# Kernel tuning notes

Measured on AMD Instinct MI355X. Metric: run time of the kernel, lower is better.

The kernel has to match this reference:

```python
import jax, jax.numpy as jnp
import numpy as np

DIM_IN, DIM_Q, DIM_V = 1024, 1024, 1024
B, S = 4, 2048
NEG_INF = 1.0e9


def setup_inputs() -> dict:
    key = jax.random.key(0)
    ks = jax.random.split(key, 11)
    c_q = (6.0 / (DIM_IN + DIM_Q)) ** 0.5
    c_v = (6.0 / (DIM_IN + DIM_V)) ** 0.5
    b_bound = 1.0 / np.sqrt(DIM_IN)  # torch Linear default bias init
    return {
        "query": jax.random.normal(ks[0], (B, S, DIM_IN), jnp.float32),
        "key": jax.random.normal(ks[1], (B, S, DIM_IN), jnp.float32),
        "value": jax.random.normal(ks[2], (B, S, DIM_IN), jnp.float32),
        "mask": jax.random.randint(ks[3], (B, S, S), 0, 2).astype(bool),
        "Wq": jax.random.uniform(ks[4], (DIM_Q, DIM_IN), jnp.float32, -c_q, c_q),
        "bq": jax.random.uniform(ks[5], (DIM_Q,), jnp.float32, -b_bound, b_bound),
        "Wk": jax.random.uniform(ks[6], (DIM_Q, DIM_IN), jnp.float32, -c_q, c_q),
        "bk": jax.random.uniform(ks[7], (DIM_Q,), jnp.float32, -b_bound, b_bound),
        "Wv": jax.random.uniform(ks[8], (DIM_V, DIM_IN), jnp.float32, -c_v, c_v),
        "bv": jax.random.uniform(ks[9], (DIM_V,), jnp.float32, -b_bound, b_bound),
    }


def reference(query, key, value, mask, Wq, bq, Wk, bk, Wv, bv):
    q = jnp.einsum("bsd,qd->bsq", query, Wq) + bq  # [B,S,dim_q]
    k = jnp.einsum("bsd,qd->bsq", key, Wk) + bk    # [B,S,dim_q]
    v = jnp.einsum("bsd,vd->bsv", value, Wv) + bv  # [B,S,dim_v]
    scale = 1.0 / jnp.sqrt(jnp.asarray(q.shape[-1], q.dtype))
    scores = jnp.einsum("bqd,bkd->bqk", q, k) * scale  # [B,S,S]
    scores = jnp.where(mask, -NEG_INF, scores)
    affinity = jax.nn.softmax(scores, axis=-1)
    out = jnp.einsum("bqk,bkv->bqv", affinity, v)  # [B,S,dim_v]
    return out
```

## Files before the change

kernel.cpp:

```cpp
#include <hip/hip_runtime.h>

#define BB 4
#define SS 2048
#define DD 1024

typedef __attribute__((ext_vector_type(8))) short short8;
typedef __attribute__((ext_vector_type(4))) float f32x4;

__device__ __forceinline__ unsigned short f2b(float f) {
  unsigned u = __builtin_bit_cast(unsigned, f);
  u += 0x7fffu + ((u >> 16) & 1u);
  return (unsigned short)(u >> 16);
}
__device__ __forceinline__ float b2f(unsigned short us) {
  unsigned u = (unsigned)us << 16;
  return __builtin_bit_cast(float, u);
}

__device__ __forceinline__ void gl2lds16(const void* g, void* l) {
  __builtin_amdgcn_global_load_lds(
      (__attribute__((address_space(1))) unsigned int*)(void*)(size_t)(uintptr_t)g,
      (__attribute__((address_space(3))) unsigned int*)l, 16, 0, 0);
}

__global__ __launch_bounds__(256) void cvt_all(
    const float* __restrict__ q, const float* __restrict__ k, const float* __restrict__ v,
    const float* __restrict__ wq, const float* __restrict__ wk, const float* __restrict__ wv,
    unsigned short* __restrict__ qo, unsigned short* __restrict__ ko, unsigned short* __restrict__ vo,
    unsigned short* __restrict__ wqo, unsigned short* __restrict__ wko, unsigned short* __restrict__ wvo) {
  const int z = blockIdx.z;
  const float* s;
  unsigned short* d;
  size_t i;
  if (blockIdx.x < 4096) {
    s = z == 0 ? q : (z == 1 ? k : v);
    d = z == 0 ? qo : (z == 1 ? ko : vo);
    i = (size_t)blockIdx.x * 2048 + threadIdx.x * 8;
  } else {
    s = z == 0 ? wq : (z == 1 ? wk : wv);
    d = z == 0 ? wqo : (z == 1 ? wko : wvo);
    i = (size_t)(blockIdx.x - 4096) * 2048 + threadIdx.x * 8;
  }
  float4 a = *(const float4*)(s + i);
  float4 b = *(const float4*)(s + i + 4);
  union { unsigned short us[8]; uint4 v4; } o;
  o.us[0] = f2b(a.x); o.us[1] = f2b(a.y); o.us[2] = f2b(a.z); o.us[3] = f2b(a.w);
  o.us[4] = f2b(b.x); o.us[5] = f2b(b.y); o.us[6] = f2b(b.z); o.us[7] = f2b(b.w);
  *(uint4*)(d + i) = o.v4;
}

enum { EPI_BIAS_COL = 0, EPI_BIAS_ROW = 1, EPI_SCORE = 2, EPI_OUT = 3 };

template <int EPI>
__global__ __launch_bounds__(256, 2) void gemm_bt(
    const unsigned short* __restrict__ A, int lda, long long aBatch,
    const unsigned short* __restrict__ Bm, int ldb, long long bBatch,
    void* __restrict__ Cv, int ldc, long long cBatch,
    int K,
    const float* __restrict__ bias,
    const float* __restrict__ bias2,
    float scale) {
  __shared__ unsigned short sA[128 * 32];
  __shared__ unsigned short sB[128 * 32];
  const int tid  = threadIdx.x;
  const int wave = tid >> 6;
  const int lane = tid & 63;
  const int l15  = lane & 15;
  const int quad = lane >> 4;
  const int waveR = wave >> 1, waveC = wave & 1;
  const int bm = blockIdx.x * 128;
  const int bn = blockIdx.y * 128;
  const int z  = blockIdx.z;
  A  += (long long)z * aBatch;
  Bm += (long long)z * bBatch;

  const unsigned short* gA0 = A  + (size_t)(bm + (tid >> 2)) * lda + (tid & 3) * 8;
  const unsigned short* gA1 = gA0 + (size_t)64 * lda;
  const unsigned short* gB0 = Bm + (size_t)(bn + (tid >> 2)) * ldb + (tid & 3) * 8;
  const unsigned short* gB1 = gB0 + (size_t)64 * ldb;
  unsigned short* lA = sA + wave * 64 * 8;
  unsigned short* lB = sB + wave * 64 * 8;

  f32x4 acc[4][4] = {};

  const int aro = (waveR * 64 + l15) * 32 + quad * 8;
  const int bro = (waveC * 64 + l15) * 32 + quad * 8;

  for (int kt = 0; kt < K; kt += 32) {
    gl2lds16(gA0, lA);
    gl2lds16(gA1, lA + 256 * 8);
    gl2lds16(gB0, lB);
    gl2lds16(gB1, lB + 256 * 8);
    gA0 += 32; gA1 += 32; gB0 += 32; gB1 += 32;
    __syncthreads();
    short8 af[4], bf[4];
#pragma unroll
    for (int i = 0; i < 4; ++i) af[i] = *(const short8*)(sA + aro + i * 16 * 32);
#pragma unroll
    for (int j = 0; j < 4; ++j) bf[j] = *(const short8*)(sB + bro + j * 16 * 32);
#pragma unroll
    for (int i = 0; i < 4; ++i)
#pragma unroll
      for (int j = 0; j < 4; ++j)
        acc[i][j] = __builtin_amdgcn_mfma_f32_16x16x32_bf16(af[i], bf[j], acc[i][j], 0, 0, 0);
    __syncthreads();
  }

  const int r0 = bm + waveR * 64 + quad * 4;
  const int c0 = bn + waveC * 64 + l15;

  if constexpr (EPI == EPI_SCORE) {
    unsigned short* Cz = (unsigned short*)Cv + (long long)z * cBatch;
#pragma unroll
    for (int i = 0; i < 4; ++i)
#pragma unroll
      for (int r = 0; r < 4; ++r) {
        int row = r0 + i * 16 + r;
#pragma unroll
        for (int j = 0; j < 4; ++j) {
          int col = c0 + j * 16;
          Cz[(size_t)row * ldc + col] = f2b(acc[i][j][r] * scale);
        }
      }
  } else if constexpr (EPI == EPI_OUT) {
    float* Cz = (float*)Cv + (long long)z * cBatch;
#pragma unroll
    for (int i = 0; i < 4; ++i)
#pragma unroll
      for (int r = 0; r < 4; ++r) {
        int row = r0 + i * 16 + r;
#pragma unroll
        for (int j = 0; j < 4; ++j) {
          int col = c0 + j * 16;
          Cz[(size_t)row * ldc + col] = acc[i][j][r];
        }
      }
  } else {
    const float* bp = (z == 0) ? bias : bias2;
    unsigned short* Cz = (unsigned short*)Cv + (long long)z * cBatch;
#pragma unroll
    for (int i = 0; i < 4; ++i)
#pragma unroll
      for (int r = 0; r < 4; ++r) {
        int row = r0 + i * 16 + r;
#pragma unroll
        for (int j = 0; j < 4; ++j) {
          int col = c0 + j * 16;
          float v = acc[i][j][r] + (EPI == EPI_BIAS_COL ? bp[col] : bp[row]);
          Cz[(size_t)row * ldc + col] = f2b(v);
        }
      }
  }
}

__global__ __launch_bounds__(256) void softmax_rows(const unsigned short* __restrict__ Sc,
                                                    const void* __restrict__ mask,
                                                    unsigned short* __restrict__ P) {
  const size_t r = blockIdx.x;
  const unsigned short* src = Sc + r * SS;
  unsigned short* dst = P + r * SS;
  const int tid = threadIdx.x;
  const int wave = tid >> 6, lane = tid & 63;
  __shared__ int anyv[4];
  __shared__ float red[8];

  unsigned pw = ((const unsigned*)mask)[tid];
  unsigned long long bal = __ballot(pw > 1u);
  if (lane == 0) anyv[wave] = (bal != 0ULL) ? 1 : 0;
  __syncthreads();
  const bool isU8 = (anyv[0] | anyv[1] | anyv[2] | anyv[3]) != 0;

  unsigned mbits = 0;
  if (isU8) {
    uint2 v = *(const uint2*)((const unsigned char*)mask + r * SS + tid * 8);
#pragma unroll
    for (int j = 0; j < 4; ++j) {
      mbits |= (((v.x >> (8 * j)) & 0xffu) ? 1u : 0u) << j;
      mbits |= (((v.y >> (8 * j)) & 0xffu) ? 1u : 0u) << (j + 4);
    }
  } else {
    const uint4* p = (const uint4*)((const int*)mask + r * SS + tid * 8);
    uint4 a = p[0], b = p[1];
    mbits = (a.x ? 1u : 0u) | ((a.y ? 1u : 0u) << 1) | ((a.z ? 1u : 0u) << 2) |
            ((a.w ? 1u : 0u) << 3) | ((b.x ? 1u : 0u) << 4) | ((b.y ? 1u : 0u) << 5) |
            ((b.z ? 1u : 0u) << 6) | ((b.w ? 1u : 0u) << 7);
  }

  union { unsigned short us[8]; uint4 v; } in;
  in.v = *(const uint4*)(src + tid * 8);
  float xs[8];
#pragma unroll
  for (int k = 0; k < 8; ++k)
    xs[k] = ((mbits >> k) & 1u) ? -1.0e9f : b2f(in.us[k]);
  float mx = xs[0];
#pragma unroll
  for (int k = 1; k < 8; ++k) mx = fmaxf(mx, xs[k]);
#pragma unroll
  for (int o = 32; o; o >>= 1) mx = fmaxf(mx, __shfl_xor(mx, o));
  if (lane == 0) red[wave] = mx;
  __syncthreads();
  mx = fmaxf(fmaxf(red[0], red[1]), fmaxf(red[2], red[3]));
  float e[8], s = 0.f;
#pragma unroll
  for (int k = 0; k < 8; ++k) { e[k] = __expf(xs[k] - mx); s += e[k]; }
#pragma unroll
  for (int o = 32; o; o >>= 1) s += __shfl_xor(s, o);
  if (lane == 0) red[4 + wave] = s;
  __syncthreads();
  s = (red[4] + red[5]) + (red[6] + red[7]);
  float inv = 1.0f / s;
  union { unsigned short us[8]; uint4 v; } o;
#pragma unroll
  for (int k = 0; k < 8; ++k) o.us[k] = f2b(e[k] * inv);
  *(uint4*)(dst + tid * 8) = o.v;
}

extern "C" void kernel_launch(void* const* d_in, const int* in_sizes, int n_in,
                              void* d_out, int out_size, void* d_ws, size_t ws_size,
                              hipStream_t stream) {
  const float* query = (const float*)d_in[0];
  const float* key   = (const float*)d_in[1];
  const float* value = (const float*)d_in[2];
  const void*  mask  = d_in[3];
  const float* Wq = (const float*)d_in[4];
  const float* bq = (const float*)d_in[5];
  const float* Wk = (const float*)d_in[6];
  const float* bk = (const float*)d_in[7];
  const float* Wv = (const float*)d_in[8];
  const float* bv = (const float*)d_in[9];
  float* out = (float*)d_out;

  char* ws = (char*)d_ws;
  const size_t MB = 1024 * 1024;
  unsigned short* qin = (unsigned short*)(ws + 0 * MB);
  unsigned short* kin = (unsigned short*)(ws + 16 * MB);
  unsigned short* vin = (unsigned short*)(ws + 32 * MB);
  unsigned short* Wqb = (unsigned short*)(ws + 48 * MB);
  unsigned short* Wkb = (unsigned short*)(ws + 50 * MB);
  unsigned short* Wvb = (unsigned short*)(ws + 52 * MB);
  unsigned short* qb  = (unsigned short*)(ws + 54 * MB);
  unsigned short* kb  = (unsigned short*)(ws + 70 * MB);
  unsigned short* vT  = (unsigned short*)(ws + 86 * MB);
  unsigned short* Sc  = (unsigned short*)(ws + 102 * MB);
  unsigned short* P   = (unsigned short*)(ws + 134 * MB);

  dim3 blk(256);

  cvt_all<<<dim3(4608, 1, 3), blk, 0, stream>>>(
      query, key, value, Wq, Wk, Wv, qin, kin, vin, Wqb, Wkb, Wvb);

  gemm_bt<EPI_BIAS_COL><<<dim3(64, 8, 2), blk, 0, stream>>>(
      qin, 1024, 8388608LL, Wqb, 1024, 1048576LL, qb, 1024, 8388608LL,
      1024, bq, bk, 0.f);

  gemm_bt<EPI_BIAS_ROW><<<dim3(8, 64, 1), blk, 0, stream>>>(
      Wvb, 1024, 0, vin, 1024, 0, vT, 8192, 0, 1024, bv, bv, 0.f);

  gemm_bt<EPI_SCORE><<<dim3(16, 16, BB), blk, 0, stream>>>(
      qb, 1024, (long long)SS * 1024, kb, 1024, (long long)SS * 1024,
      Sc, SS, (long long)SS * SS, 1024, nullptr, nullptr, 0.03125f);

  softmax_rows<<<dim3(BB * SS), blk, 0, stream>>>(Sc, mask, P);

  gemm_bt<EPI_OUT><<<dim3(16, 8, BB), blk, 0, stream>>>(
      P, SS, (long long)SS * SS, vT, 8192, (long long)SS,
      out, 1024, (long long)SS * 1024, SS, nullptr, nullptr, 1.f);
}
```

Before: 374.4 us.

## Replace 128x128 GEMM with double-buffered 256x256 tile kernel using swizzled LDS

Replaces the simple 128x128 bf16 MFMA GEMM, which syncs twice per 32-wide K step, with a 512-thread 256x256 tile kernel. It double-buffers 64-wide K tiles in 128KB of LDS, uses an XOR-swizzled LDS layout to avoid bank conflicts, and interleaves global-to-LDS staging with MFMA quadrants under explicit vmcnt waits, barriers and setprio. The goal is more data reuse per tile and overlap of memory loads with math. The cost is far fewer blocks per GEMM (for example 128 blocks for the QK projection), which may underfill the 256 CUs, plus heavy register use and 128KB of LDS per block.

```diff
diff --git a/kernel.cpp b/kernel.cpp
--- a/kernel.cpp
+++ b/kernel.cpp
@@ -51,105 +51,175 @@
 
 enum { EPI_BIAS_COL = 0, EPI_BIAS_ROW = 1, EPI_SCORE = 2, EPI_OUT = 3 };
 
+#define BAR() asm volatile("s_barrier" ::: "memory")
+#define VMW4() asm volatile("s_waitcnt vmcnt(4)" ::: "memory")
+#define VMW0() asm volatile("s_waitcnt vmcnt(0)" ::: "memory")
+
+#define MMA_QUAD(MH, NH)                                                       \
+  do {                                                                         \
+    __builtin_amdgcn_s_setprio(1);                                             \
+    _Pragma("unroll") for (int mt = 0; mt < 4; ++mt)                           \
+        _Pragma("unroll") for (int nt = 0; nt < 2; ++nt)                       \
+            _Pragma("unroll") for (int ks = 0; ks < 2; ++ks)                   \
+                acc[MH][NH][mt][nt] = __builtin_amdgcn_mfma_f32_16x16x32_bf16( \
+                    afr[mt][ks], bfr[nt][ks], acc[MH][NH][mt][nt], 0, 0, 0);   \
+    __builtin_amdgcn_s_setprio(0);                                             \
+  } while (0)
+
 template <int EPI>
-__global__ __launch_bounds__(256, 2) void gemm_bt(
+__global__ __launch_bounds__(512, 2) void gemm256(
     const unsigned short* __restrict__ A, int lda, long long aBatch,
     const unsigned short* __restrict__ Bm, int ldb, long long bBatch,
-    void* __restrict__ Cv, int ldc, long long cBatch,
-    int K,
+    void* __restrict__ Cv, int ldc, long long cBatch, int K,
     const float* __restrict__ bias,
     const float* __restrict__ bias2,
     float scale) {
-  __shared__ unsigned short sA[128 * 32];
-  __shared__ unsigned short sB[128 * 32];
-  const int tid  = threadIdx.x;
-  const int wave = tid >> 6;
-  const int lane = tid & 63;
-  const int l15  = lane & 15;
-  const int quad = lane >> 4;
-  const int waveR = wave >> 1, waveC = wave & 1;
-  const int bm = blockIdx.x * 128;
-  const int bn = blockIdx.y * 128;
-  const int z  = blockIdx.z;
-  A  += (long long)z * aBatch;
+  __shared__ __attribute__((aligned(128))) char lds[131072];
+  const int tid = threadIdx.x;
+  const int wave = tid >> 6, lane = tid & 63;
+  const int l15 = lane & 15, quad = lane >> 4;
+  const int wr = wave >> 2, wc = wave & 3;
+  const int bm = blockIdx.x * 256, bn = blockIdx.y * 256, z = blockIdx.z;
+  A += (long long)z * aBatch;
   Bm += (long long)z * bBatch;
 
-  const unsigned short* gA0 = A  + (size_t)(bm + (tid >> 2)) * lda + (tid & 3) * 8;
-  const unsigned short* gA1 = gA0 + (size_t)64 * lda;
-  const unsigned short* gB0 = Bm + (size_t)(bn + (tid >> 2)) * ldb + (tid & 3) * 8;
-  const unsigned short* gB1 = gB0 + (size_t)64 * ldb;
-  unsigned short* lA = sA + wave * 64 * 8;
-  unsigned short* lB = sB + wave * 64 * 8;
-
-  f32x4 acc[4][4] = {};
-
-  const int aro = (waveR * 64 + l15) * 32 + quad * 8;
-  const int bro = (waveC * 64 + l15) * 32 + quad * 8;
-
-  for (int kt = 0; kt < K; kt += 32) {
-    gl2lds16(gA0, lA);
-    gl2lds16(gA1, lA + 256 * 8);
-    gl2lds16(gB0, lB);
-    gl2lds16(gB1, lB + 256 * 8);
-    gA0 += 32; gA1 += 32; gB0 += 32; gB1 += 32;
-    __syncthreads();
-    short8 af[4], bf[4];
-#pragma unroll
-    for (int i = 0; i < 4; ++i) af[i] = *(const short8*)(sA + aro + i * 16 * 32);
-#pragma unroll
-    for (int j = 0; j < 4; ++j) bf[j] = *(const short8*)(sB + bro + j * 16 * 32);
-#pragma unroll
-    for (int i = 0; i < 4; ++i)
-#pragma unroll
-      for (int j = 0; j < 4; ++j)
-        acc[i][j] = __builtin_amdgcn_mfma_f32_16x16x32_bf16(af[i], bf[j], acc[i][j], 0, 0, 0);
-    __syncthreads();
-  }
-
-  const int r0 = bm + waveR * 64 + quad * 4;
-  const int c0 = bn + waveC * 64 + l15;
-
+  const int laneterm = l15 * 64 + ((quad * 16) ^ ((l15 & 8) << 2));
+
+  size_t aoff0, aoff1, boff0, boff1;
+  int dst0, dst1;
+  {
+    int s = tid, s2 = s ^ (((s >> 5) & 1) << 1);
+    int row = (s2 >> 7) * 16 + ((s2 >> 2) & 15);
+    int col = ((s2 >> 6) & 1) * 32 + (s2 & 3) * 8;
+    aoff0 = (size_t)(bm + row) * lda + col;
+    boff0 = (size_t)(bn + row) * ldb + col;
+    dst0 = (tid & ~63) * 16;
+    s = tid + 512; s2 = s ^ (((s >> 5) & 1) << 1);
+    row = (s2 >> 7) * 16 + ((s2 >> 2) & 15);
+    col = ((s2 >> 6) & 1) * 32 + (s2 & 3) * 8;
+    aoff1 = (size_t)(bm + row) * lda + col;
+    boff1 = (size_t)(bn + row) * ldb + col;
+    dst1 = (tid & ~63) * 16 + 8192;
+  }
+
+  auto stageA = [&](int buf, int half, int t) {
+    const unsigned short* s0 = A + aoff0 + (size_t)(half * 128) * lda + t * 64;
+    const unsigned short* s1 = A + aoff1 + (size_t)(half * 128) * lda + t * 64;
+    char* d = lds + buf * 65536 + half * 16384;
+    gl2lds16(s0, d + dst0);
+    gl2lds16(s1, d + dst1);
+  };
+  auto stageB = [&](int buf, int half, int t) {
+    const unsigned short* s0 = Bm + boff0 + (size_t)(half * 128) * ldb + t * 64;
+    const unsigned short* s1 = Bm + boff1 + (size_t)(half * 128) * ldb + t * 64;
+    char* d = lds + 32768 + buf * 65536 + half * 16384;
+    gl2lds16(s0, d + dst0);
+    gl2lds16(s1, d + dst1);
+  };
+
+  f32x4 acc[2][2][4][2] = {};
+  short8 afr[4][2], bfr[2][2];
+
+  auto loadA = [&](int buf, int mh) {
+    const char* rg = lds + buf * 65536 + mh * 16384;
+#pragma unroll
+    for (int mt = 0; mt < 4; ++mt)
+#pragma unroll
+      for (int ks = 0; ks < 2; ++ks)
+        afr[mt][ks] = *(const short8*)(rg + ((wr * 4 + mt) * 2 + ks) * 1024 + laneterm);
+  };
+  auto loadB = [&](int buf, int nh) {
+    const char* rg = lds + 32768 + buf * 65536 + nh * 16384;
+#pragma unroll
+    for (int nt = 0; nt < 2; ++nt)
+#pragma unroll
+      for (int ks = 0; ks < 2; ++ks)
+        bfr[nt][ks] = *(const short8*)(rg + ((wc * 2 + nt) * 2 + ks) * 1024 + laneterm);
+  };
+
+  const int NT = K >> 6;
+  const int NI = NT >> 1;
+
+  stageA(0, 0, 0); stageA(0, 1, 0); stageB(0, 0, 0); stageB(0, 1, 0);
+  stageA(1, 0, 1); stageB(1, 0, 1);
+  VMW4(); BAR();
+
+  for (int i = 0; i < NI - 1; ++i) {
+    const int t1 = 2 * i + 1;
+    loadA(0, 0); loadB(0, 0); stageA(1, 1, t1);              BAR(); MMA_QUAD(0, 0); BAR();
+    loadB(0, 1);              stageB(1, 1, t1);              BAR(); MMA_QUAD(0, 1); BAR();
+    loadA(0, 1); loadB(0, 0); stageA(0, 0, t1 + 1);          BAR(); MMA_QUAD(1, 0); BAR();
+    loadB(0, 1);              stageB(0, 0, t1 + 1); VMW4();  BAR(); MMA_QUAD(1, 1); BAR();
+    loadA(1, 0); loadB(1, 0); stageA(0, 1, t1 + 1);          BAR(); MMA_QUAD(0, 0); BAR();
+    loadB(1, 1);              stageB(0, 1, t1 + 1);          BAR(); MMA_QUAD(0, 1); BAR();
+    loadA(1, 1); loadB(1, 0); stageA(1, 0, t1 + 2);          BAR(); MMA_QUAD(1, 0); BAR();
+    loadB(1, 1);              stageB(1, 0, t1 + 2); VMW4();  BAR(); MMA_QUAD(1, 1); BAR();
+  }
+  {
+    const int t1 = NT - 1;
+    loadA(0, 0); loadB(0, 0); stageA(1, 1, t1);              BAR(); MMA_QUAD(0, 0); BAR();
+    loadB(0, 1);              stageB(1, 1, t1);              BAR(); MMA_QUAD(0, 1); BAR();
+    loadA(0, 1); loadB(0, 0);                                BAR(); MMA_QUAD(1, 0); BAR();
+    loadB(0, 1);                                    VMW0();  BAR(); MMA_QUAD(1, 1); BAR();
+    loadA(1, 0); loadB(1, 0);                                BAR(); MMA_QUAD(0, 0); BAR();
+    loadB(1, 1);                                             BAR(); MMA_QUAD(0, 1); BAR();
+    loadA(1, 1); loadB(1, 0);                                BAR(); MMA_QUAD(1, 0); BAR();
+    loadB(1, 1);                                             BAR(); MMA_QUAD(1, 1);
+  }
+
+  const int r0 = bm + wr * 64 + quad * 4;
+  const int c0 = bn + wc * 32 + l15;
   if constexpr (EPI == EPI_SCORE) {
     unsigned short* Cz = (unsigned short*)Cv + (long long)z * cBatch;
 #pragma unroll
-    for (int i = 0; i < 4; ++i)
-#pragma unroll
-      for (int r = 0; r < 4; ++r) {
-        int row = r0 + i * 16 + r;
-#pragma unroll
-        for (int j = 0; j < 4; ++j) {
-          int col = c0 + j * 16;
-          Cz[(size_t)row * ldc + col] = f2b(acc[i][j][r] * scale);
+    for (int mh = 0; mh < 2; ++mh)
+#pragma unroll
+      for (int mt = 0; mt < 4; ++mt)
+#pragma unroll
+        for (int r = 0; r < 4; ++r) {
+          const int row = r0 + mh * 128 + mt * 16 + r;
+#pragma unroll
+          for (int nh = 0; nh < 2; ++nh)
+#pragma unroll
+            for (int nt = 0; nt < 2; ++nt)
+              Cz[(size_t)row * ldc + c0 + nh * 128 + nt * 16] =
+                  f2b(acc[mh][nh][mt][nt][r] * scale);
         }
-      }
   } else if constexpr (EPI == EPI_OUT) {
     float* Cz = (float*)Cv + (long long)z * cBatch;
 #pragma unroll
-    for (int i = 0; i < 4; ++i)
-#pragma unroll
-      for (int r = 0; r < 4; ++r) {
-        int row = r0 + i * 16 + r;
-#pragma unroll
-        for (int j = 0; j < 4; ++j) {
-          int col = c0 + j * 16;
-          Cz[(size_t)row * ldc + col] = acc[i][j][r];
+    for (int mh = 0; mh < 2; ++mh)
+#pragma unroll
+      for (int mt = 0; mt < 4; ++mt)
+#pragma unroll
+        for (int r = 0; r < 4; ++r) {
+          const int row = r0 + mh * 128 + mt * 16 + r;
+#pragma unroll
+          for (int nh = 0; nh < 2; ++nh)
+#pragma unroll
+            for (int nt = 0; nt < 2; ++nt)
+              Cz[(size_t)row * ldc + c0 + nh * 128 + nt * 16] = acc[mh][nh][mt][nt][r];
         }
-      }
   } else {
     const float* bp = (z == 0) ? bias : bias2;
     unsigned short* Cz = (unsigned short*)Cv + (long long)z * cBatch;
 #pragma unroll
-    for (int i = 0; i < 4; ++i)
-#pragma unroll
-      for (int r = 0; r < 4; ++r) {
-        int row = r0 + i * 16 + r;
-#pragma unroll
-        for (int j = 0; j < 4; ++j) {
-          int col = c0 + j * 16;
-          float v = acc[i][j][r] + (EPI == EPI_BIAS_COL ? bp[col] : bp[row]);
-          Cz[(size_t)row * ldc + col] = f2b(v);
+    for (int mh = 0; mh < 2; ++mh)
+#pragma unroll
+      for (int mt = 0; mt < 4; ++mt)
+#pragma unroll
+        for (int r = 0; r < 4; ++r) {
+          const int row = r0 + mh * 128 + mt * 16 + r;
+#pragma unroll
+          for (int nh = 0; nh < 2; ++nh)
+#pragma unroll
+            for (int nt = 0; nt < 2; ++nt) {
+              const int col = c0 + nh * 128 + nt * 16;
+              float v = acc[mh][nh][mt][nt][r] +
+                        (EPI == EPI_BIAS_COL ? bp[col] : bp[row]);
+              Cz[(size_t)row * ldc + col] = f2b(v);
+            }
         }
-      }
   }
 }
 
@@ -244,25 +314,25 @@
   unsigned short* Sc  = (unsigned short*)(ws + 102 * MB);
   unsigned short* P   = (unsigned short*)(ws + 134 * MB);
 
-  dim3 blk(256);
+  dim3 blk(256), blk512(512);
 
   cvt_all<<<dim3(4608, 1, 3), blk, 0, stream>>>(
       query, key, value, Wq, Wk, Wv, qin, kin, vin, Wqb, Wkb, Wvb);
 
-  gemm_bt<EPI_BIAS_COL><<<dim3(64, 8, 2), blk, 0, stream>>>(
+  gemm256<EPI_BIAS_COL><<<dim3(32, 4, 2), blk512, 0, stream>>>(
       qin, 1024, 8388608LL, Wqb, 1024, 1048576LL, qb, 1024, 8388608LL,
       1024, bq, bk, 0.f);
 
-  gemm_bt<EPI_BIAS_ROW><<<dim3(8, 64, 1), blk, 0, stream>>>(
+  gemm256<EPI_BIAS_ROW><<<dim3(4, 32, 1), blk512, 0, stream>>>(
       Wvb, 1024, 0, vin, 1024, 0, vT, 8192, 0, 1024, bv, bv, 0.f);
 
-  gemm_bt<EPI_SCORE><<<dim3(16, 16, BB), blk, 0, stream>>>(
+  gemm256<EPI_SCORE><<<dim3(8, 8, BB), blk512, 0, stream>>>(
       qb, 1024, (long long)SS * 1024, kb, 1024, (long long)SS * 1024,
       Sc, SS, (long long)SS * SS, 1024, nullptr, nullptr, 0.03125f);
 
   softmax_rows<<<dim3(BB * SS), blk, 0, stream>>>(Sc, mask, P);
 
-  gemm_bt<EPI_OUT><<<dim3(16, 8, BB), blk, 0, stream>>>(
+  gemm256<EPI_OUT><<<dim3(8, 4, BB), blk512, 0, stream>>>(
       P, SS, (long long)SS * SS, vT, 8192, (long long)SS,
       out, 1024, (long long)SS * 1024, SS, nullptr, nullptr, 1.f);
 }
```

Result: faster. 365.1 us (-2.5%).

## Double-buffer GEMM LDS tiles and merge Q/K/V projections into one launch

Applied to the files above, without the earlier changes.

Turns the shared GEMM main loop into a two-stage LDS double buffer. The next K-tile's global-to-LDS loads are issued after the current fragments are read and before the MFMAs, with one barrier per iteration instead of two. The three projection GEMMs are also merged into a single proj_all launch so the V projection runs alongside Q and K. LDS use per block doubles, which may limit occupancy, and the correctness of the single-barrier scheme relies on the async load ordering.

```diff
diff --git a/kernel.cpp b/kernel.cpp
--- a/kernel.cpp
+++ b/kernel.cpp
@@ -49,65 +49,105 @@
   *(uint4*)(d + i) = o.v4;
 }
 
-enum { EPI_BIAS_COL = 0, EPI_BIAS_ROW = 1, EPI_SCORE = 2, EPI_OUT = 3 };
+#define GEMM_BODY(A_, lda_, B_, ldb_, KK)                                       \
+  __shared__ unsigned short sA[2][128 * 32];                                    \
+  __shared__ unsigned short sB[2][128 * 32];                                    \
+  const int tid  = threadIdx.x;                                                 \
+  const int wave = tid >> 6;                                                    \
+  const int lane = tid & 63;                                                    \
+  const int l15  = lane & 15;                                                   \
+  const int quad = lane >> 4;                                                   \
+  const int waveR = wave >> 1, waveC = wave & 1;                                \
+  const unsigned short* gA0 = A_ + (size_t)(bm + (tid >> 2)) * lda_ + (tid & 3) * 8; \
+  const unsigned short* gA1 = gA0 + (size_t)64 * lda_;                          \
+  const unsigned short* gB0 = B_ + (size_t)(bn + (tid >> 2)) * ldb_ + (tid & 3) * 8; \
+  const unsigned short* gB1 = gB0 + (size_t)64 * ldb_;                          \
+  const int ldsOff = wave * 64 * 8;                                             \
+  f32x4 acc[4][4] = {};                                                         \
+  const int aro = (waveR * 64 + l15) * 32 + quad * 8;                           \
+  const int bro = (waveC * 64 + l15) * 32 + quad * 8;                           \
+  auto stage = [&](int c, int kt) {                                             \
+    unsigned short* lA = sA[c] + ldsOff;                                        \
+    unsigned short* lB = sB[c] + ldsOff;                                        \
+    gl2lds16(gA0 + kt, lA);                                                     \
+    gl2lds16(gA1 + kt, lA + 256 * 8);                                           \
+    gl2lds16(gB0 + kt, lB);                                                     \
+    gl2lds16(gB1 + kt, lB + 256 * 8);                                           \
+  };                                                                            \
+  stage(0, 0);                                                                  \
+  int cur = 0;                                                                  \
+  for (int kt = 0; kt < (KK); kt += 32) {                                       \
+    __syncthreads();                                                            \
+    short8 af[4], bf[4];                                                        \
+    _Pragma("unroll")                                                           \
+    for (int i = 0; i < 4; ++i) af[i] = *(const short8*)(sA[cur] + aro + i * 16 * 32); \
+    _Pragma("unroll")                                                           \
+    for (int j = 0; j < 4; ++j) bf[j] = *(const short8*)(sB[cur] + bro + j * 16 * 32); \
+    __builtin_amdgcn_sched_barrier(0);                                          \
+    if (kt + 32 < (KK)) stage(cur ^ 1, kt + 32);                                \
+    __builtin_amdgcn_sched_barrier(0);                                          \
+    _Pragma("unroll")                                                           \
+    for (int i = 0; i < 4; ++i)                                                 \
+      _Pragma("unroll")                                                         \
+      for (int j = 0; j < 4; ++j)                                               \
+        acc[i][j] = __builtin_amdgcn_mfma_f32_16x16x32_bf16(af[i], bf[j], acc[i][j], 0, 0, 0); \
+    cur ^= 1;                                                                   \
+  }                                                                             \
+  const int r0 = bm + waveR * 64 + quad * 4;                                    \
+  const int c0 = bn + waveC * 64 + l15;
+
+__global__ __launch_bounds__(256, 2) void proj_all(
+    const unsigned short* __restrict__ qin, const unsigned short* __restrict__ kin,
+    const unsigned short* __restrict__ vin,
+    const unsigned short* __restrict__ Wqb, const unsigned short* __restrict__ Wkb,
+    const unsigned short* __restrict__ Wvb,
+    const float* __restrict__ bq, const float* __restrict__ bk,
+    const float* __restrict__ bv,
+    unsigned short* __restrict__ qkb,
+    unsigned short* __restrict__ vT) {
+  const int z = blockIdx.z;
+  const unsigned short *Ap, *Bp; const float* bp;
+  unsigned short* C; int ldc, bm, bn; bool rowb;
+  if (z == 2) {
+    Ap = Wvb; Bp = vin; bp = bv; C = vT; ldc = 8192; rowb = true;
+    bm = blockIdx.y * 128; bn = blockIdx.x * 128;
+  } else {
+    Ap = z ? kin : qin; Bp = z ? Wkb : Wqb; bp = z ? bk : bq;
+    C = qkb + (size_t)z * 8388608; ldc = 1024; rowb = false;
+    bm = blockIdx.x * 128; bn = blockIdx.y * 128;
+  }
+
+  GEMM_BODY(Ap, 1024, Bp, 1024, 1024)
+
+#pragma unroll
+  for (int i = 0; i < 4; ++i)
+#pragma unroll
+    for (int r = 0; r < 4; ++r) {
+      int row = r0 + i * 16 + r;
+#pragma unroll
+      for (int j = 0; j < 4; ++j) {
+        int col = c0 + j * 16;
+        float v = acc[i][j][r] + (rowb ? bp[row] : bp[col]);
+        C[(size_t)row * ldc + col] = f2b(v);
+      }
+    }
+}
+
+enum { EPI_SCORE = 2, EPI_OUT = 3 };
 
 template <int EPI>
 __global__ __launch_bounds__(256, 2) void gemm_bt(
     const unsigned short* __restrict__ A, int lda, long long aBatch,
     const unsigned short* __restrict__ Bm, int ldb, long long bBatch,
     void* __restrict__ Cv, int ldc, long long cBatch,
-    int K,
-    const float* __restrict__ bias,
-    const float* __restrict__ bias2,
-    float scale) {
-  __shared__ unsigned short sA[128 * 32];
-  __shared__ unsigned short sB[128 * 32];
-  const int tid  = threadIdx.x;
-  const int wave = tid >> 6;
-  const int lane = tid & 63;
-  const int l15  = lane & 15;
-  const int quad = lane >> 4;
-  const int waveR = wave >> 1, waveC = wave & 1;
+    int K, float scale) {
   const int bm = blockIdx.x * 128;
   const int bn = blockIdx.y * 128;
   const int z  = blockIdx.z;
-  A  += (long long)z * aBatch;
-  Bm += (long long)z * bBatch;
-
-  const unsigned short* gA0 = A  + (size_t)(bm + (tid >> 2)) * lda + (tid & 3) * 8;
-  const unsigned short* gA1 = gA0 + (size_t)64 * lda;
-  const unsigned short* gB0 = Bm + (size_t)(bn + (tid >> 2)) * ldb + (tid & 3) * 8;
-  const unsigned short* gB1 = gB0 + (size_t)64 * ldb;
-  unsigned short* lA = sA + wave * 64 * 8;
-  unsigned short* lB = sB + wave * 64 * 8;
-
-  f32x4 acc[4][4] = {};
-
-  const int aro = (waveR * 64 + l15) * 32 + quad * 8;
-  const int bro = (waveC * 64 + l15) * 32 + quad * 8;
-
-  for (int kt = 0; kt < K; kt += 32) {
-    gl2lds16(gA0, lA);
-    gl2lds16(gA1, lA + 256 * 8);
-    gl2lds16(gB0, lB);
-    gl2lds16(gB1, lB + 256 * 8);
-    gA0 += 32; gA1 += 32; gB0 += 32; gB1 += 32;
-    __syncthreads();
-    short8 af[4], bf[4];
-#pragma unroll
-    for (int i = 0; i < 4; ++i) af[i] = *(const short8*)(sA + aro + i * 16 * 32);
-#pragma unroll
-    for (int j = 0; j < 4; ++j) bf[j] = *(const short8*)(sB + bro + j * 16 * 32);
-#pragma unroll
-    for (int i = 0; i < 4; ++i)
-#pragma unroll
-      for (int j = 0; j < 4; ++j)
-        acc[i][j] = __builtin_amdgcn_mfma_f32_16x16x32_bf16(af[i], bf[j], acc[i][j], 0, 0, 0);
-    __syncthreads();
-  }
-
-  const int r0 = bm + waveR * 64 + quad * 4;
-  const int c0 = bn + waveC * 64 + l15;
+  const unsigned short* Az = A  + (long long)z * aBatch;
+  const unsigned short* Bz = Bm + (long long)z * bBatch;
+
+  GEMM_BODY(Az, lda, Bz, ldb, K)
 
   if constexpr (EPI == EPI_SCORE) {
     unsigned short* Cz = (unsigned short*)Cv + (long long)z * cBatch;
@@ -122,7 +162,7 @@
           Cz[(size_t)row * ldc + col] = f2b(acc[i][j][r] * scale);
         }
       }
-  } else if constexpr (EPI == EPI_OUT) {
+  } else {
     float* Cz = (float*)Cv + (long long)z * cBatch;
 #pragma unroll
     for (int i = 0; i < 4; ++i)
@@ -133,21 +173,6 @@
         for (int j = 0; j < 4; ++j) {
           int col = c0 + j * 16;
           Cz[(size_t)row * ldc + col] = acc[i][j][r];
-        }
-      }
-  } else {
-    const float* bp = (z == 0) ? bias : bias2;
-    unsigned short* Cz = (unsigned short*)Cv + (long long)z * cBatch;
-#pragma unroll
-    for (int i = 0; i < 4; ++i)
-#pragma unroll
-      for (int r = 0; r < 4; ++r) {
-        int row = r0 + i * 16 + r;
-#pragma unroll
-        for (int j = 0; j < 4; ++j) {
-          int col = c0 + j * 16;
-          float v = acc[i][j][r] + (EPI == EPI_BIAS_COL ? bp[col] : bp[row]);
-          Cz[(size_t)row * ldc + col] = f2b(v);
         }
       }
   }
@@ -249,20 +274,16 @@
   cvt_all<<<dim3(4608, 1, 3), blk, 0, stream>>>(
       query, key, value, Wq, Wk, Wv, qin, kin, vin, Wqb, Wkb, Wvb);
 
-  gemm_bt<EPI_BIAS_COL><<<dim3(64, 8, 2), blk, 0, stream>>>(
-      qin, 1024, 8388608LL, Wqb, 1024, 1048576LL, qb, 1024, 8388608LL,
-      1024, bq, bk, 0.f);
-
-  gemm_bt<EPI_BIAS_ROW><<<dim3(8, 64, 1), blk, 0, stream>>>(
-      Wvb, 1024, 0, vin, 1024, 0, vT, 8192, 0, 1024, bv, bv, 0.f);
+  proj_all<<<dim3(64, 8, 3), blk, 0, stream>>>(
+      qin, kin, vin, Wqb, Wkb, Wvb, bq, bk, bv, qb, vT);
 
   gemm_bt<EPI_SCORE><<<dim3(16, 16, BB), blk, 0, stream>>>(
       qb, 1024, (long long)SS * 1024, kb, 1024, (long long)SS * 1024,
-      Sc, SS, (long long)SS * SS, 1024, nullptr, nullptr, 0.03125f);
+      Sc, SS, (long long)SS * SS, 1024, 0.03125f);
 
   softmax_rows<<<dim3(BB * SS), blk, 0, stream>>>(Sc, mask, P);
 
   gemm_bt<EPI_OUT><<<dim3(16, 8, BB), blk, 0, stream>>>(
       P, SS, (long long)SS * SS, vT, 8192, (long long)SS,
-      out, 1024, (long long)SS * 1024, SS, nullptr, nullptr, 1.f);
-}
+      out, 1024, (long long)SS * 1024, SS, 1.f);
+}
```

Result: faster. 356.8 us (-4.7%).
